# Optimization experiments

Hardware: AMD Instinct MI355X
Metric: run time of the kernel (lower is better)

The kernel has to match this reference:

```python
import jax, jax.numpy as jnp
import numpy as np

N = 4096
TOPK = 16
LEAKY = 0.2
LN_EPS = 1e-5


def _gat(x, W, a_s, a_d, b, src, dst, heads):
    # PyG-style GATConv (self-loops already included in src/dst).
    n = x.shape[0]
    h = (x @ W).reshape(n, heads, -1)                      # [N,H,F]
    e = jax.nn.leaky_relu((h * a_s).sum(-1)[src] + (h * a_d).sum(-1)[dst], LEAKY)  # [E,H]
    m = jax.ops.segment_max(e, dst, num_segments=n)        # segment softmax over dst
    p = jnp.exp(e - m[dst])
    s = jax.ops.segment_sum(p, dst, num_segments=n)
    alpha = p / s[dst]                                     # [E,H]
    out = jax.ops.segment_sum(alpha[:, :, None] * h[src], dst, num_segments=n)  # [N,H,F]
    return out.reshape(n, -1) + b


def _ln(x, g, b):
    mu = x.mean(-1, keepdims=True)
    v = ((x - mu) ** 2).mean(-1, keepdims=True)
    return (x - mu) / jnp.sqrt(v + LN_EPS) * g + b


def _transformer_layer(x, wqkv, bqkv, wo, bo, g1, b1g, w1, bb1, w2, bb2, g2, b2g, nhead):
    n, d = x.shape
    dh = d // nhead
    qkv = x @ wqkv.T + bqkv                                # [N,3d]
    q, k, v = jnp.split(qkv, 3, axis=-1)
    q = q.reshape(n, nhead, dh)
    k = k.reshape(n, nhead, dh)
    v = v.reshape(n, nhead, dh)
    scores = jnp.einsum('nhd,mhd->hnm', q, k) / jnp.sqrt(jnp.float32(dh))
    attn = jax.nn.softmax(scores, axis=-1)
    o = jnp.einsum('hnm,mhd->nhd', attn, v).reshape(n, d)
    x = _ln(x + (o @ wo.T + bo), g1, b1g)
    ff = jax.nn.relu(x @ w1 + bb1) @ w2 + bb2
    return _ln(x + ff, g2, b2g)


def _learn_graph(window, gl_w, gl_b):
    h = jnp.tanh(window @ gl_w + gl_b)                     # [N,hid]
    sim = h @ h.T                                          # [N,N]
    adj = jax.nn.relu(sim)
    masked = jnp.where(jnp.eye(N, dtype=bool), -1e9, adj)  # exclude self in top-k
    _, idx = jax.lax.top_k(masked, TOPK)                   # [N,TOPK]
    src = idx.reshape(-1)
    dst = jnp.repeat(jnp.arange(N), TOPK)
    loop = jnp.arange(N)
    return jnp.concatenate([src, loop]), jnp.concatenate([dst, loop])


def setup_inputs() -> dict:
    key = jax.random.key(0)
    ks = iter(jax.random.split(key, 64))
    def rn(shape, s=0.05):
        return jax.random.normal(next(ks), shape, jnp.float32) * s
    d = dict(
        window=rn((N, 256), 1.0),
        gl_w=rn((256, 256)), gl_b=rn((256,)),
        enc_W=rn((3, 256, 256)), enc_asrc=rn((3, 4, 64)), enc_adst=rn((3, 4, 64)), enc_b=rn((3, 256)),
        tr_wqkv=rn((2, 768, 256)), tr_bqkv=rn((2, 768)),
        tr_wo=rn((2, 256, 256)), tr_bo=rn((2, 256)),
        tr_ln1_g=jnp.ones((2, 256), jnp.float32), tr_ln1_b=jnp.zeros((2, 256), jnp.float32),
        tr_w1=rn((2, 256, 512)), tr_b1=rn((2, 512)),
        tr_w2=rn((2, 512, 256)), tr_b2=rn((2, 256)),
        tr_ln2_g=jnp.ones((2, 256), jnp.float32), tr_ln2_b=jnp.zeros((2, 256), jnp.float32),
        skip_w=rn((256, 256)), skip_b=rn((256,)),
        dec_W=rn((2, 256, 256)), dec_asrc=rn((2, 4, 64)), dec_adst=rn((2, 4, 64)), dec_b=rn((2, 256)),
        dec_lW=rn((256, 256)), dec_lasrc=rn((1, 1, 256)), dec_ladst=rn((1, 1, 256)), dec_lb=rn((256,)),
    )
    return d


def reference(window, gl_w, gl_b, enc_W, enc_asrc, enc_adst, enc_b,
              tr_wqkv, tr_bqkv, tr_wo, tr_bo, tr_ln1_g, tr_ln1_b,
              tr_w1, tr_b1, tr_w2, tr_b2, tr_ln2_g, tr_ln2_b,
              skip_w, skip_b, dec_W, dec_asrc, dec_adst, dec_b,
              dec_lW, dec_lasrc, dec_ladst, dec_lb):
    src, dst = _learn_graph(window, gl_w, gl_b)
    # encoder: 3 GAT layers with ReLU
    x = window
    for i in range(3):
        x = jax.nn.relu(_gat(x, enc_W[i], enc_asrc[i], enc_adst[i], enc_b[i], src, dst, 4))
    # transformer bottleneck (batch of 1 sequence of N tokens)
    h = x
    for i in range(2):
        h = _transformer_layer(h, tr_wqkv[i], tr_bqkv[i], tr_wo[i], tr_bo[i],
                               tr_ln1_g[i], tr_ln1_b[i], tr_w1[i], tr_b1[i],
                               tr_w2[i], tr_b2[i], tr_ln2_g[i], tr_ln2_b[i], 4)
    # skip connection
    h = h + (window @ skip_w + skip_b)
    # decoder: 2 GAT layers with ReLU, then single-head GAT
    x = h
    for i in range(2):
        x = jax.nn.relu(_gat(x, dec_W[i], dec_asrc[i], dec_adst[i], dec_b[i], src, dst, 4))
    out = _gat(x, dec_lW, dec_lasrc[0], dec_ladst[0], dec_lb, src, dst, 1)
    return out.T
```

## Files before the change

kernel.cpp:

```cpp
#include <hip/hip_runtime.h>
#include <math.h>

#define NN 4096
#define DM 256

enum { ACT_NONE = 0, ACT_RELU = 1, ACT_TANH = 2 };

typedef __attribute__((ext_vector_type(8))) short short8v;
typedef __attribute__((ext_vector_type(16))) float f32x16;

__device__ __forceinline__ unsigned short f2bf(float f) {
  unsigned int u = __float_as_uint(f);
  unsigned int r = (u + 0x7FFFu + ((u >> 16) & 1u)) >> 16;
  return (unsigned short)r;
}
__device__ __forceinline__ float bf2f(unsigned short u) {
  return __uint_as_float(((unsigned int)u) << 16);
}

__global__ __launch_bounds__(256) void cast_k(
    const float* __restrict__ src, unsigned short* __restrict__ dst, int n4) {
  const int i = blockIdx.x * 256 + threadIdx.x;
  if (i < n4) {
    const float4 v = ((const float4*)src)[i];
    ushort4 u;
    u.x = f2bf(v.x); u.y = f2bf(v.y); u.z = f2bf(v.z); u.w = f2bf(v.w);
    ((ushort4*)dst)[i] = u;
  }
}

__global__ __launch_bounds__(256) void tcast_k(
    const float* __restrict__ src, unsigned short* __restrict__ dst, int K, int N) {
  __shared__ float tile[32][33];
  const int n0 = blockIdx.x * 32, k0 = blockIdx.y * 32;
  const int tx = threadIdx.x & 31, ty = threadIdx.x >> 5;
#pragma unroll
  for (int r2 = 0; r2 < 4; r2++)
    tile[ty + r2 * 8][tx] = src[(size_t)(k0 + ty + r2 * 8) * N + n0 + tx];
  __syncthreads();
#pragma unroll
  for (int r2 = 0; r2 < 4; r2++)
    dst[(size_t)(n0 + ty + r2 * 8) * K + k0 + tx] = f2bf(tile[tx][ty + r2 * 8]);
}

__global__ __launch_bounds__(256) void split_k(
    const float* __restrict__ h, unsigned short* __restrict__ Aext,
    unsigned short* __restrict__ Bext) {
  const int n = blockIdx.x, t = threadIdx.x;
  const float v = h[(size_t)n * DM + t];
  const unsigned short hi = f2bf(v);
  const unsigned short lo = f2bf(v - bf2f(hi));
  unsigned short* ar = Aext + (size_t)n * 768;
  unsigned short* br = Bext + (size_t)n * 768;
  ar[t] = hi; ar[256 + t] = lo; ar[512 + t] = hi;
  br[t] = hi; br[256 + t] = hi; br[512 + t] = lo;
}

template<bool BT, int ACT, bool BIAS, bool RES>
__global__ __launch_bounds__(256) void gemm_k(
    const float* __restrict__ A, const float* __restrict__ B,
    const float* __restrict__ bias, const float* __restrict__ res,
    float* __restrict__ C, int M, int N, int K) {
  __shared__ float As[16][64];
  __shared__ float Bs[16][64];
  const int t = threadIdx.x;
  const int tx = t & 15, ty = t >> 4;
  const int m0 = blockIdx.y * 64, n0 = blockIdx.x * 64;
  float acc[4][4];
#pragma unroll
  for (int i = 0; i < 4; i++)
#pragma unroll
    for (int j = 0; j < 4; j++) acc[i][j] = 0.f;

  const int i_ld = t >> 2, kq = t & 3;
  for (int k0 = 0; k0 < K; k0 += 16) {
    float4 a4 = *(const float4*)(A + (size_t)(m0 + i_ld) * K + k0 + kq * 4);
    As[kq * 4 + 0][i_ld] = a4.x; As[kq * 4 + 1][i_ld] = a4.y;
    As[kq * 4 + 2][i_ld] = a4.z; As[kq * 4 + 3][i_ld] = a4.w;
    if (BT) {
      float4 b4 = *(const float4*)(B + (size_t)(n0 + i_ld) * K + k0 + kq * 4);
      Bs[kq * 4 + 0][i_ld] = b4.x; Bs[kq * 4 + 1][i_ld] = b4.y;
      Bs[kq * 4 + 2][i_ld] = b4.z; Bs[kq * 4 + 3][i_ld] = b4.w;
    } else {
      const int kk = t >> 4, j4 = (t & 15) * 4;
      float4 b4 = *(const float4*)(B + (size_t)(k0 + kk) * N + n0 + j4);
      *(float4*)&Bs[kk][j4] = b4;
    }
    __syncthreads();
#pragma unroll
    for (int kk = 0; kk < 16; kk++) {
      const float4 av = *(const float4*)&As[kk][ty * 4];
      const float4 bv = *(const float4*)&Bs[kk][tx * 4];
      acc[0][0] += av.x * bv.x; acc[0][1] += av.x * bv.y;
      acc[0][2] += av.x * bv.z; acc[0][3] += av.x * bv.w;
      acc[1][0] += av.y * bv.x; acc[1][1] += av.y * bv.y;
      acc[1][2] += av.y * bv.z; acc[1][3] += av.y * bv.w;
      acc[2][0] += av.z * bv.x; acc[2][1] += av.z * bv.y;
      acc[2][2] += av.z * bv.z; acc[2][3] += av.z * bv.w;
      acc[3][0] += av.w * bv.x; acc[3][1] += av.w * bv.y;
      acc[3][2] += av.w * bv.z; acc[3][3] += av.w * bv.w;
    }
    __syncthreads();
  }
  const int n = n0 + tx * 4;
#pragma unroll
  for (int i = 0; i < 4; i++) {
    const int m = m0 + ty * 4 + i;
    float4 v = make_float4(acc[i][0], acc[i][1], acc[i][2], acc[i][3]);
    if (BIAS) {
      v.x += bias[n + 0]; v.y += bias[n + 1];
      v.z += bias[n + 2]; v.w += bias[n + 3];
    }
    if (RES) {
      const float4 rv = *(const float4*)(res + (size_t)m * N + n);
      v.x += rv.x; v.y += rv.y; v.z += rv.z; v.w += rv.w;
    }
    if (ACT == ACT_RELU) {
      v.x = fmaxf(v.x, 0.f); v.y = fmaxf(v.y, 0.f);
      v.z = fmaxf(v.z, 0.f); v.w = fmaxf(v.w, 0.f);
    } else if (ACT == ACT_TANH) {
      v.x = tanhf(v.x); v.y = tanhf(v.y); v.z = tanhf(v.z); v.w = tanhf(v.w);
    }
    *(float4*)(C + (size_t)m * N + n) = v;
  }
}

template<int ACT, bool BIAS, bool RES, bool F32OUT, bool B16OUT>
__global__ __launch_bounds__(256) void mgemm_k(
    const unsigned short* __restrict__ A, const unsigned short* __restrict__ Bt,
    const float* __restrict__ bias, const float* __restrict__ res,
    float* __restrict__ C, unsigned short* __restrict__ Cb,
    int M, int N, int K) {
  __shared__ short As[64][64];
  __shared__ short Bs[64][64];
  const int t = threadIdx.x;
  const int m0 = blockIdx.y * 64, n0 = blockIdx.x * 64;
  const int wid = t >> 6, l = t & 63, l31 = l & 31, g = l >> 5;
  const int wm = wid >> 1, wn = wid & 1;
  f32x16 acc;
#pragma unroll
  for (int r = 0; r < 16; r++) acc[r] = 0.f;

  for (int k0 = 0; k0 < K; k0 += 64) {
#pragma unroll
    for (int p = 0; p < 2; p++) {
      const int j = p * 256 + t, row = j >> 3, ch = j & 7, sch = ch ^ (row & 7);
      *(short8v*)&As[row][sch * 8] =
          *(const short8v*)((const short*)A + (size_t)(m0 + row) * K + k0 + ch * 8);
      *(short8v*)&Bs[row][sch * 8] =
          *(const short8v*)((const short*)Bt + (size_t)(n0 + row) * K + k0 + ch * 8);
    }
    __syncthreads();
#pragma unroll
    for (int ck = 0; ck < 4; ck++) {
      const int c = ck * 2 + g;
      const short8v af = *(const short8v*)&As[wm * 32 + l31][(c ^ (l31 & 7)) * 8];
      const short8v bf = *(const short8v*)&Bs[wn * 32 + l31][(c ^ (l31 & 7)) * 8];
      acc = __builtin_amdgcn_mfma_f32_32x32x16_bf16(bf, af, acc, 0, 0, 0);
    }
    __syncthreads();
  }
  const int m = m0 + wm * 32 + l31;
#pragma unroll
  for (int b = 0; b < 4; b++) {
    const int n = n0 + wn * 32 + b * 8 + g * 4;
    float4 v = make_float4(acc[b * 4 + 0], acc[b * 4 + 1],
                           acc[b * 4 + 2], acc[b * 4 + 3]);
    if (BIAS) {
      v.x += bias[n + 0]; v.y += bias[n + 1];
      v.z += bias[n + 2]; v.w += bias[n + 3];
    }
    if (RES) {
      const float4 rv = *(const float4*)(res + (size_t)m * N + n);
      v.x += rv.x; v.y += rv.y; v.z += rv.z; v.w += rv.w;
    }
    if (ACT == ACT_RELU) {
      v.x = fmaxf(v.x, 0.f); v.y = fmaxf(v.y, 0.f);
      v.z = fmaxf(v.z, 0.f); v.w = fmaxf(v.w, 0.f);
    }
    if (F32OUT) *(float4*)(C + (size_t)m * N + n) = v;
    if (B16OUT) {
      ushort4 uv;
      uv.x = f2bf(v.x); uv.y = f2bf(v.y); uv.z = f2bf(v.z); uv.w = f2bf(v.w);
      *(ushort4*)(Cb + (size_t)m * N + n) = uv;
    }
  }
}

__global__ __launch_bounds__(256) void topk16_k(
    const float* __restrict__ sim, int* __restrict__ idxo, int rowbase) {
  const int r = blockIdx.x, t = threadIdx.x;
  const int grow = rowbase + r;
  float val[16];
#pragma unroll
  for (int q = 0; q < 16; q++) {
    const int jj = q * 256 + t;
    float v = sim[(size_t)r * NN + jj];
    v = fmaxf(v, 0.f);
    if (jj == grow) v = -1.f;
    val[q] = v;
  }
  __shared__ float cv[64];
  __shared__ int cjs[64];
  const int wave = t >> 6, lane = t & 63;
  float myv = -3.f; int myj = 0;
  for (int it = 0; it < 16; it++) {
    float bv = -10.f; int bj = 0;
#pragma unroll
    for (int q = 0; q < 16; q++)
      if (val[q] > bv) { bv = val[q]; bj = q * 256 + t; }
#pragma unroll
    for (int off = 1; off < 64; off <<= 1) {
      const float ov = __shfl_xor(bv, off);
      const int oj = __shfl_xor(bj, off);
      if (ov > bv || (ov == bv && oj < bj)) { bv = ov; bj = oj; }
    }
    if (lane == it) { myv = bv; myj = bj; }
    if ((bj & 255) == t) {
      const int q = bj >> 8;
#pragma unroll
      for (int qq = 0; qq < 16; qq++) if (qq == q) val[qq] = -2.f;
    }
  }
  if (lane < 16) { cv[wave * 16 + lane] = myv; cjs[wave * 16 + lane] = myj; }
  __syncthreads();
  if (wave == 0) {
    float bv2 = cv[lane]; int bj2 = cjs[lane];
    for (int it = 0; it < 16; it++) {
      float wv = bv2; int wj = bj2;
#pragma unroll
      for (int off = 1; off < 64; off <<= 1) {
        const float ov = __shfl_xor(wv, off);
        const int oj = __shfl_xor(wj, off);
        if (ov > wv || (ov == wv && oj < wj)) { wv = ov; wj = oj; }
      }
      if (lane == 0) idxo[(size_t)grow * 16 + it] = wj;
      if (wj == bj2) bv2 = -3.f;
    }
  }
}

template<int H>
__global__ __launch_bounds__(256) void gat_prep_k(
    const float* __restrict__ h, const float* __restrict__ as,
    const float* __restrict__ ad, float* __restrict__ es, float* __restrict__ ed) {
  __shared__ float bs[4], bd[4];
  const int n = blockIdx.x, t = threadIdx.x;
  const float v = h[(size_t)n * DM + t];
  float ps = v * as[t];
  float pd = v * ad[t];
#pragma unroll
  for (int off = 32; off >= 1; off >>= 1) {
    ps += __shfl_down(ps, off, 64);
    pd += __shfl_down(pd, off, 64);
  }
  const int wave = t >> 6, lane = t & 63;
  if (H == 4) {
    if (lane == 0) { es[n * 4 + wave] = ps; ed[n * 4 + wave] = pd; }
  } else {
    if (lane == 0) { bs[wave] = ps; bd[wave] = pd; }
    __syncthreads();
    if (t == 0) {
      es[n] = bs[0] + bs[1] + bs[2] + bs[3];
      ed[n] = bd[0] + bd[1] + bd[2] + bd[3];
    }
  }
}

template<int H, bool RELU, bool B16OUT>
__global__ __launch_bounds__(256) void gat_aggr_k(
    const float* __restrict__ h, const float* __restrict__ es,
    const float* __restrict__ ed, const int* __restrict__ idx,
    const float* __restrict__ bias, float* __restrict__ out,
    unsigned short* __restrict__ outb) {
  const int j = blockIdx.x, t = threadIdx.x;
  const int hd = (H == 4) ? (t >> 6) : 0;
  __shared__ int srcs[17];
  if (t < 16) srcs[t] = idx[(size_t)j * 16 + t];
  if (t == 16) srcs[16] = j;
  __syncthreads();
  const float edj = ed[j * H + hd];
  float e[17]; float m = -1e30f;
#pragma unroll
  for (int k = 0; k < 17; k++) {
    float ev = es[srcs[k] * H + hd] + edj;
    ev = (ev >= 0.f) ? ev : 0.2f * ev;
    e[k] = ev; m = fmaxf(m, ev);
  }
  float s = 0.f;
#pragma unroll
  for (int k = 0; k < 17; k++) { e[k] = expf(e[k] - m); s += e[k]; }
  const float inv = 1.f / s;
  float acc = 0.f;
#pragma unroll
  for (int k = 0; k < 17; k++) acc += e[k] * h[(size_t)srcs[k] * DM + t];
  acc = acc * inv + bias[t];
  if (RELU) acc = fmaxf(acc, 0.f);
  out[(size_t)j * DM + t] = acc;
  if (B16OUT) outb[(size_t)j * DM + t] = f2bf(acc);
}

__global__ __launch_bounds__(256) void vtrans_k(
    const short* __restrict__ qkvs, short* __restrict__ vt) {
  __shared__ short Vt[64][72];
  const int kb0 = blockIdx.x * 64;
  const int h = blockIdx.y;
  const int t = threadIdx.x;
  {
    const int key = t >> 2, cq = t & 3;
    const short* vp = qkvs + (size_t)(kb0 + key) * 768 + 512 + h * 64 + cq * 16;
    *(short8v*)&Vt[key][cq * 16] = *(const short8v*)(vp);
    *(short8v*)&Vt[key][cq * 16 + 8] = *(const short8v*)(vp + 8);
  }
  __syncthreads();
  const int dh = t & 63, grp = t >> 6;
  short* dst = vt + (size_t)(h * 64 + dh) * 4096 + kb0 + grp * 16;
#pragma unroll
  for (int j2 = 0; j2 < 2; j2++) {
    short8v tmp;
#pragma unroll
    for (int e = 0; e < 8; e++) {
      const int s = grp * 16 + j2 * 8 + e;
      const int w = (s & 32) | ((s & 19)) | ((s & 4) << 1) | ((s & 8) >> 1);
      tmp[e] = Vt[w][dh];
    }
    *(short8v*)(dst + j2 * 8) = tmp;
  }
}

#define LOADKV(KF, VF, KB) do {                                               \
    const short* kp_ = kbase + (size_t)((KB) + l31) * 768;                    \
    KF##0 = *(const short8v*)(kp_);                                           \
    KF##1 = *(const short8v*)(kp_ + 16);                                      \
    KF##2 = *(const short8v*)(kp_ + 32);                                      \
    KF##3 = *(const short8v*)(kp_ + 48);                                      \
    const short* vp_ = vbase + (KB);                                          \
    VF##0 = *(const short8v*)(vp_);                                           \
    VF##1 = *(const short8v*)(vp_ + 16);                                      \
    VF##2 = *(const short8v*)(vp_ + (size_t)32 * 4096);                       \
    VF##3 = *(const short8v*)(vp_ + (size_t)32 * 4096 + 16);                  \
  } while (0)

#define PROCESS(KF, VF) do {                                                  \
    f32x16 accS;                                                              \
    _Pragma("unroll") for (int r = 0; r < 16; r++) accS[r] = 0.f;             \
    __builtin_amdgcn_s_setprio(1);                                            \
    accS = __builtin_amdgcn_mfma_f32_32x32x16_bf16(KF##0, qf[0], accS, 0, 0, 0); \
    accS = __builtin_amdgcn_mfma_f32_32x32x16_bf16(KF##1, qf[1], accS, 0, 0, 0); \
    accS = __builtin_amdgcn_mfma_f32_32x32x16_bf16(KF##2, qf[2], accS, 0, 0, 0); \
    accS = __builtin_amdgcn_mfma_f32_32x32x16_bf16(KF##3, qf[3], accS, 0, 0, 0); \
    __builtin_amdgcn_s_setprio(0);                                            \
    float sv[16]; float mt = -1e30f;                                          \
    _Pragma("unroll") for (int r = 0; r < 16; r++) {                          \
      sv[r] = accS[r] * 0.18033688f;                     \
      mt = fmaxf(mt, sv[r]);                                                  \
    }                                                                         \
    mt = fmaxf(mt, __shfl_xor(mt, 32));                                       \
    float pv[16]; float ls = 0.f;                                             \
    if (__all(mt <= mrun + 11.5416f)) {                                       \
      _Pragma("unroll") for (int r = 0; r < 16; r++) {                        \
        pv[r] = exp2f(sv[r] - mrun); ls += pv[r];                             \
      }                                                                       \
      ls += __shfl_xor(ls, 32); lrun += ls;                                   \
    } else {                                                                  \
      const float mnew = fmaxf(mrun, mt);                                     \
      const float corr = exp2f(mrun - mnew);                                  \
      _Pragma("unroll") for (int r = 0; r < 16; r++) {                        \
        pv[r] = exp2f(sv[r] - mnew); ls += pv[r];                             \
      }                                                                       \
      ls += __shfl_xor(ls, 32);                                               \
      lrun = lrun * corr + ls; mrun = mnew;                                   \
      _Pragma("unroll") for (int r = 0; r < 16; r++) {                        \
        accO[0][r] *= corr; accO[1][r] *= corr;                               \
      }                                                                       \
    }                                                                         \
    union { unsigned int u[8]; short8v s[2]; } pf;                            \
    _Pragma("unroll") for (int r = 0; r < 8; r++) {                           \
      unsigned int po;                                                        \
      asm("v_cvt_pk_bf16_f32 %0, %1, %2"                                      \
          : "=v"(po) : "v"(pv[2 * r]), "v"(pv[2 * r + 1]));                   \
      pf.u[r] = po;                                                           \
    }                                                                         \
    __builtin_amdgcn_s_setprio(1);                                            \
    accO[0] = __builtin_amdgcn_mfma_f32_32x32x16_bf16(VF##0, pf.s[0], accO[0], 0, 0, 0); \
    accO[0] = __builtin_amdgcn_mfma_f32_32x32x16_bf16(VF##1, pf.s[1], accO[0], 0, 0, 0); \
    accO[1] = __builtin_amdgcn_mfma_f32_32x32x16_bf16(VF##2, pf.s[0], accO[1], 0, 0, 0); \
    accO[1] = __builtin_amdgcn_mfma_f32_32x32x16_bf16(VF##3, pf.s[1], accO[1], 0, 0, 0); \
    __builtin_amdgcn_s_setprio(0);                                            \
  } while (0)

__global__ __launch_bounds__(64) void attn_flash_k(
    const short* __restrict__ qkvs, const short* __restrict__ vt,
    unsigned short* __restrict__ opart, float* __restrict__ ml) {
  const int qb = blockIdx.x * 32;
  const int h = blockIdx.y;
  const int z = blockIdx.z;
  const int l = threadIdx.x;
  const int l31 = l & 31, g = l >> 5;

  short8v qf[4];
  {
    const short* qp = qkvs + (size_t)(qb + l31) * 768 + h * 64 + g * 8;
#pragma unroll
    for (int c = 0; c < 4; c++) qf[c] = *(const short8v*)(qp + c * 16);
  }

  f32x16 accO[2];
#pragma unroll
  for (int r = 0; r < 16; r++) { accO[0][r] = 0.f; accO[1][r] = 0.f; }
  float mrun = -1e30f, lrun = 0.f;

  const short* kbase = qkvs + 256 + h * 64 + g * 8;
  const short* vbase = vt + (size_t)(h * 64 + l31) * 4096 + g * 8;
  const int kb0 = z * 1024;

  short8v kA0, kA1, kA2, kA3, vA0, vA1, vA2, vA3;
  short8v kB0, kB1, kB2, kB3, vB0, vB1, vB2, vB3;
  LOADKV(kA, vA, kb0);
  for (int it = 0; it < 16; it++) {
    LOADKV(kB, vB, kb0 + (it * 2 + 1) * 32);
    PROCESS(kA, vA);
    LOADKV(kA, vA, kb0 + ((it * 2 + 2) & 31) * 32);
    PROCESS(kB, vB);
  }

  const int q = qb + l31;
  unsigned short* op = opart + ((size_t)z * NN + q) * DM + h * 64;
#pragma unroll
  for (int db = 0; db < 2; db++) {
#pragma unroll
    for (int rq = 0; rq < 4; rq++) {
      ushort4 v4;
      v4.x = f2bf(accO[db][rq * 4 + 0]);
      v4.y = f2bf(accO[db][rq * 4 + 1]);
      v4.z = f2bf(accO[db][rq * 4 + 2]);
      v4.w = f2bf(accO[db][rq * 4 + 3]);
      *(ushort4*)(op + db * 32 + rq * 8 + g * 4) = v4;
    }
  }
  if (g == 0) {
    ml[(((size_t)z * 4 + h) * NN + q) * 2 + 0] = mrun;
    ml[(((size_t)z * 4 + h) * NN + q) * 2 + 1] = lrun;
  }
}

__global__ __launch_bounds__(256) void attn_merge_k(
    const unsigned short* __restrict__ opart, const float* __restrict__ ml,
    unsigned short* __restrict__ ob) {
  const int q = blockIdx.x;
  const int t = threadIdx.x;
  const int h = t >> 6;
  float m[4], lv[4];
#pragma unroll
  for (int z = 0; z < 4; z++) {
    m[z]  = ml[(((size_t)z * 4 + h) * NN + q) * 2 + 0];
    lv[z] = ml[(((size_t)z * 4 + h) * NN + q) * 2 + 1];
  }
  const float ms = fmaxf(fmaxf(m[0], m[1]), fmaxf(m[2], m[3]));
  float w[4]; float ls = 0.f;
#pragma unroll
  for (int z = 0; z < 4; z++) {
    w[z] = exp2f(m[z] - ms);
    ls += lv[z] * w[z];
  }
  const float inv = 1.f / ls;
  float acc = 0.f;
#pragma unroll
  for (int z = 0; z < 4; z++)
    acc += bf2f(opart[((size_t)z * NN + q) * DM + t]) * w[z];
  ob[(size_t)q * DM + t] = f2bf(acc * inv);
}

__global__ __launch_bounds__(256) void ln_k(
    const float* __restrict__ x, const float* __restrict__ g,
    const float* __restrict__ b, float* __restrict__ y,
    unsigned short* __restrict__ yb) {
  __shared__ float bs[4], bs2[4];
  const int n = blockIdx.x, t = threadIdx.x;
  const float v = x[(size_t)n * DM + t];
  float s = v, s2 = v * v;
#pragma unroll
  for (int off = 32; off >= 1; off >>= 1) {
    s += __shfl_down(s, off, 64);
    s2 += __shfl_down(s2, off, 64);
  }
  const int wave = t >> 6, lane = t & 63;
  if (lane == 0) { bs[wave] = s; bs2[wave] = s2; }
  __syncthreads();
  const float ts = bs[0] + bs[1] + bs[2] + bs[3];
  const float ts2 = bs2[0] + bs2[1] + bs2[2] + bs2[3];
  const float mu = ts * (1.f / 256.f);
  const float var = ts2 * (1.f / 256.f) - mu * mu;
  const float rstd = 1.f / sqrtf(var + 1e-5f);
  const float o = (v - mu) * rstd * g[t] + b[t];
  y[(size_t)n * DM + t] = o;
  yb[(size_t)n * DM + t] = f2bf(o);
}

__global__ __launch_bounds__(1024) void transpose_k(
    const float* __restrict__ x, float* __restrict__ out) {
  __shared__ float tile[32][33];
  const int n0 = blockIdx.x * 32, c0 = blockIdx.y * 32;
  const int tx = threadIdx.x, ty = threadIdx.y;
  tile[ty][tx] = x[(size_t)(n0 + ty) * DM + c0 + tx];
  __syncthreads();
  out[(size_t)(c0 + ty) * NN + n0 + tx] = tile[tx][ty];
}

extern "C" void kernel_launch(void* const* d_in, const int* in_sizes, int n_in,
                              void* d_out, int out_size, void* d_ws, size_t ws_size,
                              hipStream_t stream) {
  (void)in_sizes; (void)n_in; (void)out_size; (void)ws_size;
  const float* window   = (const float*)d_in[0];
  const float* gl_w     = (const float*)d_in[1];
  const float* gl_b     = (const float*)d_in[2];
  const float* enc_W    = (const float*)d_in[3];
  const float* enc_asrc = (const float*)d_in[4];
  const float* enc_adst = (const float*)d_in[5];
  const float* enc_b    = (const float*)d_in[6];
  const float* tr_wqkv  = (const float*)d_in[7];
  const float* tr_bqkv  = (const float*)d_in[8];
  const float* tr_wo    = (const float*)d_in[9];
  const float* tr_bo    = (const float*)d_in[10];
  const float* tr_ln1_g = (const float*)d_in[11];
  const float* tr_ln1_b = (const float*)d_in[12];
  const float* tr_w1    = (const float*)d_in[13];
  const float* tr_b1    = (const float*)d_in[14];
  const float* tr_w2    = (const float*)d_in[15];
  const float* tr_b2    = (const float*)d_in[16];
  const float* tr_ln2_g = (const float*)d_in[17];
  const float* tr_ln2_b = (const float*)d_in[18];
  const float* skip_w   = (const float*)d_in[19];
  const float* skip_b   = (const float*)d_in[20];
  const float* dec_W    = (const float*)d_in[21];
  const float* dec_asrc = (const float*)d_in[22];
  const float* dec_adst = (const float*)d_in[23];
  const float* dec_b    = (const float*)d_in[24];
  const float* dec_lW   = (const float*)d_in[25];
  const float* dec_lasrc= (const float*)d_in[26];
  const float* dec_ladst= (const float*)d_in[27];
  const float* dec_lb   = (const float*)d_in[28];
  float* outp = (float*)d_out;

  float* ws   = (float*)d_ws;
  float* xa   = ws;
  float* xb   = ws + 1048576;
  float* hp   = ws + 2097152;
  float* t1   = ws + 3145728;
  float* hgl  = t1;
  float* mlb  = t1;
  float* qkvb = ws + 4194304;
  float* vtb  = ws + 5767168;
  float* Rg   = ws + 6291456;
  float* simc = Rg;
  unsigned short* opartb = (unsigned short*)Rg;
  unsigned short* ffb    = (unsigned short*)Rg;
  float* es   = ws + 8388608;
  float* ed   = ws + 8404992;
  int*   idx  = (int*)(ws + 8421376);
  unsigned short* winb = (unsigned short*)(ws + 8486912);
  unsigned short* actb = (unsigned short*)(ws + 9011200);
  unsigned short* wb   = (unsigned short*)(ws + 9535488);

  unsigned short* encWt = wb;
  unsigned short* wqkvb = wb + 196608;
  unsigned short* wob   = wb + 589824;
  unsigned short* w1t   = wb + 720896;
  unsigned short* w2t   = wb + 983040;
  unsigned short* skipt = wb + 1245184;
  unsigned short* dect  = wb + 1310720;
  unsigned short* declt = wb + 1441792;

  unsigned short* Aext = (unsigned short*)qkvb;
  unsigned short* Bext = (unsigned short*)xa;

  const dim3 B256(256);

  cast_k<<<dim3(1024), B256, 0, stream>>>(window, winb, 262144);
  for (int i = 0; i < 3; i++)
    tcast_k<<<dim3(8, 8), B256, 0, stream>>>(enc_W + (size_t)i * 65536, encWt + (size_t)i * 65536, 256, 256);
  cast_k<<<dim3(384), B256, 0, stream>>>(tr_wqkv, wqkvb, 98304);
  cast_k<<<dim3(128), B256, 0, stream>>>(tr_wo, wob, 32768);
  for (int i = 0; i < 2; i++) {
    tcast_k<<<dim3(16, 8), B256, 0, stream>>>(tr_w1 + (size_t)i * 131072, w1t + (size_t)i * 131072, 256, 512);
    tcast_k<<<dim3(8, 16), B256, 0, stream>>>(tr_w2 + (size_t)i * 131072, w2t + (size_t)i * 131072, 512, 256);
    tcast_k<<<dim3(8, 8), B256, 0, stream>>>(dec_W + (size_t)i * 65536, dect + (size_t)i * 65536, 256, 256);
  }
  tcast_k<<<dim3(8, 8), B256, 0, stream>>>(skip_w, skipt, 256, 256);
  tcast_k<<<dim3(8, 8), B256, 0, stream>>>(dec_lW, declt, 256, 256);

  gemm_k<false, ACT_TANH, true, false><<<dim3(DM / 64, NN / 64), B256, 0, stream>>>(
      window, gl_w, gl_b, nullptr, hgl, NN, DM, DM);

  split_k<<<dim3(NN), B256, 0, stream>>>(hgl, Aext, Bext);
  for (int c = 0; c < 8; c++) {
    mgemm_k<ACT_NONE, false, false, true, false><<<dim3(64, 8), B256, 0, stream>>>(
        Aext + (size_t)c * 512 * 768, Bext, nullptr, nullptr, simc, nullptr,
        512, NN, 768);
    topk16_k<<<dim3(512), B256, 0, stream>>>(simc, idx, c * 512);
  }

  for (int i = 0; i < 3; i++) {
    const unsigned short* ain = (i == 0) ? winb : actb;
    mgemm_k<ACT_NONE, false, false, true, false><<<dim3(4, 64), B256, 0, stream>>>(
        ain, encWt + (size_t)i * 65536, nullptr, nullptr, hp, nullptr, NN, DM, DM);
    gat_prep_k<4><<<dim3(NN), B256, 0, stream>>>(hp, enc_asrc + i * 256, enc_adst + i * 256, es, ed);
    gat_aggr_k<4, true, true><<<dim3(NN), B256, 0, stream>>>(
        hp, es, ed, idx, enc_b + i * 256, xa, actb);
  }

  for (int i = 0; i < 2; i++) {
    mgemm_k<ACT_NONE, true, false, false, true><<<dim3(12, 64), B256, 0, stream>>>(
        actb, wqkvb + (size_t)i * 196608, tr_bqkv + i * 768, nullptr,
        nullptr, (unsigned short*)qkvb, NN, 768, DM);
    vtrans_k<<<dim3(64, 4), B256, 0, stream>>>((const short*)qkvb, (short*)vtb);
    attn_flash_k<<<dim3(NN / 32, 4, 4), dim3(64), 0, stream>>>(
        (const short*)qkvb, (const short*)vtb, opartb, mlb);
    attn_merge_k<<<dim3(NN), B256, 0, stream>>>(opartb, mlb, actb);
    mgemm_k<ACT_NONE, true, true, true, false><<<dim3(4, 64), B256, 0, stream>>>(
        actb, wob + (size_t)i * 65536, tr_bo + i * 256, xa, t1, nullptr, NN, DM, DM);
    ln_k<<<dim3(NN), B256, 0, stream>>>(t1, tr_ln1_g + i * 256, tr_ln1_b + i * 256, xb, actb);
    mgemm_k<ACT_RELU, true, false, false, true><<<dim3(8, 64), B256, 0, stream>>>(
        actb, w1t + (size_t)i * 131072, tr_b1 + i * 512, nullptr,
        nullptr, ffb, NN, 512, DM);
    mgemm_k<ACT_NONE, true, true, true, false><<<dim3(4, 64), B256, 0, stream>>>(
        ffb, w2t + (size_t)i * 131072, tr_b2 + i * 256, xb, t1, nullptr, NN, DM, 512);
    ln_k<<<dim3(NN), B256, 0, stream>>>(t1, tr_ln2_g + i * 256, tr_ln2_b + i * 256, xa, actb);
  }

  mgemm_k<ACT_NONE, true, true, false, true><<<dim3(4, 64), B256, 0, stream>>>(
      winb, skipt, skip_b, xa, nullptr, actb, NN, DM, DM);

  mgemm_k<ACT_NONE, false, false, true, false><<<dim3(4, 64), B256, 0, stream>>>(
      actb, dect, nullptr, nullptr, hp, nullptr, NN, DM, DM);
  gat_prep_k<4><<<dim3(NN), B256, 0, stream>>>(hp, dec_asrc, dec_adst, es, ed);
  gat_aggr_k<4, true, true><<<dim3(NN), B256, 0, stream>>>(hp, es, ed, idx, dec_b, xb, actb);

  mgemm_k<ACT_NONE, false, false, true, false><<<dim3(4, 64), B256, 0, stream>>>(
      actb, dect + 65536, nullptr, nullptr, hp, nullptr, NN, DM, DM);
  gat_prep_k<4><<<dim3(NN), B256, 0, stream>>>(hp, dec_asrc + 256, dec_adst + 256, es, ed);
  gat_aggr_k<4, true, true><<<dim3(NN), B256, 0, stream>>>(hp, es, ed, idx, dec_b + 256, xb, actb);

  mgemm_k<ACT_NONE, false, false, true, false><<<dim3(4, 64), B256, 0, stream>>>(
      actb, declt, nullptr, nullptr, hp, nullptr, NN, DM, DM);
  gat_prep_k<1><<<dim3(NN), B256, 0, stream>>>(hp, dec_lasrc, dec_ladst, es, ed);
  gat_aggr_k<1, false, false><<<dim3(NN), B256, 0, stream>>>(hp, es, ed, idx, dec_lb, xa, nullptr);

  transpose_k<<<dim3(NN / 32, DM / 32), dim3(32, 32), 0, stream>>>(xa, outp);
}
```

Measured before the change: 857.0 us.

## Merge flash-attention split-K partials in shared memory and batch weight casts

The attention kernel now runs 8 waves per block, each handling a 512-key slice, and merges their partial outputs and softmax stats through shared memory. This removes the separate merge kernel and the global round trip of the bf16 partials. The softmax scale is folded into Q when it is loaded, which drops a multiply per score but rounds the scaled Q to bf16 once more. The many cast/transpose launches for weights are also batched into two launches. The cost is heavier shared-memory use and block-wide synchronisation inside the attention kernel.

```diff
diff --git a/kernel.cpp b/kernel.cpp
--- a/kernel.cpp
+++ b/kernel.cpp
@@ -18,29 +18,33 @@
   return __uint_as_float(((unsigned int)u) << 16);
 }
 
-__global__ __launch_bounds__(256) void cast_k(
-    const float* __restrict__ src, unsigned short* __restrict__ dst, int n4) {
+struct CastJob { const float* s; unsigned short* d; int n4; };
+__global__ __launch_bounds__(256) void castall_k(CastJob j0, CastJob j1, CastJob j2) {
+  const CastJob* jp = (blockIdx.y == 0) ? &j0 : (blockIdx.y == 1) ? &j1 : &j2;
   const int i = blockIdx.x * 256 + threadIdx.x;
-  if (i < n4) {
-    const float4 v = ((const float4*)src)[i];
+  if (i < jp->n4) {
+    const float4 v = ((const float4*)jp->s)[i];
     ushort4 u;
     u.x = f2bf(v.x); u.y = f2bf(v.y); u.z = f2bf(v.z); u.w = f2bf(v.w);
-    ((ushort4*)dst)[i] = u;
-  }
-}
-
-__global__ __launch_bounds__(256) void tcast_k(
-    const float* __restrict__ src, unsigned short* __restrict__ dst, int K, int N) {
+    ((ushort4*)jp->d)[i] = u;
+  }
+}
+
+struct TJob { const float* s; unsigned short* d; int K; int N; };
+struct TJobs { TJob j[11]; };
+__global__ __launch_bounds__(256) void tcastall_k(TJobs js) {
+  const TJob jb = js.j[blockIdx.z];
+  const int n0 = blockIdx.x * 32, k0 = blockIdx.y * 32;
+  if (n0 >= jb.N || k0 >= jb.K) return;
   __shared__ float tile[32][33];
-  const int n0 = blockIdx.x * 32, k0 = blockIdx.y * 32;
   const int tx = threadIdx.x & 31, ty = threadIdx.x >> 5;
 #pragma unroll
   for (int r2 = 0; r2 < 4; r2++)
-    tile[ty + r2 * 8][tx] = src[(size_t)(k0 + ty + r2 * 8) * N + n0 + tx];
+    tile[ty + r2 * 8][tx] = jb.s[(size_t)(k0 + ty + r2 * 8) * jb.N + n0 + tx];
   __syncthreads();
 #pragma unroll
   for (int r2 = 0; r2 < 4; r2++)
-    dst[(size_t)(n0 + ty + r2 * 8) * K + k0 + tx] = f2bf(tile[tx][ty + r2 * 8]);
+    jb.d[(size_t)(n0 + ty + r2 * 8) * jb.K + k0 + tx] = f2bf(tile[tx][ty + r2 * 8]);
 }
 
 __global__ __launch_bounds__(256) void split_k(
@@ -350,23 +354,20 @@
     accS = __builtin_amdgcn_mfma_f32_32x32x16_bf16(KF##2, qf[2], accS, 0, 0, 0); \
     accS = __builtin_amdgcn_mfma_f32_32x32x16_bf16(KF##3, qf[3], accS, 0, 0, 0); \
     __builtin_amdgcn_s_setprio(0);                                            \
-    float sv[16]; float mt = -1e30f;                                          \
-    _Pragma("unroll") for (int r = 0; r < 16; r++) {                          \
-      sv[r] = accS[r] * 0.18033688f;                     \
-      mt = fmaxf(mt, sv[r]);                                                  \
-    }                                                                         \
+    float mt = -1e30f;                                                        \
+    _Pragma("unroll") for (int r = 0; r < 16; r++) mt = fmaxf(mt, accS[r]);   \
     mt = fmaxf(mt, __shfl_xor(mt, 32));                                       \
     float pv[16]; float ls = 0.f;                                             \
     if (__all(mt <= mrun + 11.5416f)) {                                       \
       _Pragma("unroll") for (int r = 0; r < 16; r++) {                        \
-        pv[r] = exp2f(sv[r] - mrun); ls += pv[r];                             \
+        pv[r] = exp2f(accS[r] - mrun); ls += pv[r];                           \
       }                                                                       \
       ls += __shfl_xor(ls, 32); lrun += ls;                                   \
     } else {                                                                  \
       const float mnew = fmaxf(mrun, mt);                                     \
       const float corr = exp2f(mrun - mnew);                                  \
       _Pragma("unroll") for (int r = 0; r < 16; r++) {                        \
-        pv[r] = exp2f(sv[r] - mnew); ls += pv[r];                             \
+        pv[r] = exp2f(accS[r] - mnew); ls += pv[r];                           \
       }                                                                       \
       ls += __shfl_xor(ls, 32);                                               \
       lrun = lrun * corr + ls; mrun = mnew;                                   \
@@ -389,20 +390,30 @@
     __builtin_amdgcn_s_setprio(0);                                            \
   } while (0)
 
-__global__ __launch_bounds__(64) void attn_flash_k(
+__global__ __launch_bounds__(512, 4) void attn_flash_k(
     const short* __restrict__ qkvs, const short* __restrict__ vt,
-    unsigned short* __restrict__ opart, float* __restrict__ ml) {
+    unsigned short* __restrict__ ob) {
   const int qb = blockIdx.x * 32;
   const int h = blockIdx.y;
-  const int z = blockIdx.z;
-  const int l = threadIdx.x;
+  const int t = threadIdx.x;
+  const int w = t >> 6;
+  const int l = t & 63;
   const int l31 = l & 31, g = l >> 5;
+
+  __shared__ float smem[8][32][66];
+  __shared__ float sml[8][32][2];
 
   short8v qf[4];
   {
     const short* qp = qkvs + (size_t)(qb + l31) * 768 + h * 64 + g * 8;
 #pragma unroll
-    for (int c = 0; c < 4; c++) qf[c] = *(const short8v*)(qp + c * 16);
+    for (int c = 0; c < 4; c++) {
+      short8v qv = *(const short8v*)(qp + c * 16);
+#pragma unroll
+      for (int e = 0; e < 8; e++)
+        qv[e] = (short)f2bf(bf2f((unsigned short)qv[e]) * 0.18033688f);
+      qf[c] = qv;
+    }
   }
 
   f32x16 accO[2];
@@ -412,63 +423,53 @@
 
   const short* kbase = qkvs + 256 + h * 64 + g * 8;
   const short* vbase = vt + (size_t)(h * 64 + l31) * 4096 + g * 8;
-  const int kb0 = z * 1024;
+  const int kb0 = w * 512;
 
   short8v kA0, kA1, kA2, kA3, vA0, vA1, vA2, vA3;
   short8v kB0, kB1, kB2, kB3, vB0, vB1, vB2, vB3;
   LOADKV(kA, vA, kb0);
-  for (int it = 0; it < 16; it++) {
+  for (int it = 0; it < 8; it++) {
     LOADKV(kB, vB, kb0 + (it * 2 + 1) * 32);
     PROCESS(kA, vA);
-    LOADKV(kA, vA, kb0 + ((it * 2 + 2) & 31) * 32);
+    LOADKV(kA, vA, kb0 + ((it * 2 + 2) & 15) * 32);
     PROCESS(kB, vB);
   }
 
-  const int q = qb + l31;
-  unsigned short* op = opart + ((size_t)z * NN + q) * DM + h * 64;
-#pragma unroll
-  for (int db = 0; db < 2; db++) {
-#pragma unroll
-    for (int rq = 0; rq < 4; rq++) {
-      ushort4 v4;
-      v4.x = f2bf(accO[db][rq * 4 + 0]);
-      v4.y = f2bf(accO[db][rq * 4 + 1]);
-      v4.z = f2bf(accO[db][rq * 4 + 2]);
-      v4.w = f2bf(accO[db][rq * 4 + 3]);
-      *(ushort4*)(op + db * 32 + rq * 8 + g * 4) = v4;
-    }
-  }
-  if (g == 0) {
-    ml[(((size_t)z * 4 + h) * NN + q) * 2 + 0] = mrun;
-    ml[(((size_t)z * 4 + h) * NN + q) * 2 + 1] = lrun;
-  }
-}
-
-__global__ __launch_bounds__(256) void attn_merge_k(
-    const unsigned short* __restrict__ opart, const float* __restrict__ ml,
-    unsigned short* __restrict__ ob) {
-  const int q = blockIdx.x;
-  const int t = threadIdx.x;
-  const int h = t >> 6;
-  float m[4], lv[4];
-#pragma unroll
-  for (int z = 0; z < 4; z++) {
-    m[z]  = ml[(((size_t)z * 4 + h) * NN + q) * 2 + 0];
-    lv[z] = ml[(((size_t)z * 4 + h) * NN + q) * 2 + 1];
-  }
-  const float ms = fmaxf(fmaxf(m[0], m[1]), fmaxf(m[2], m[3]));
-  float w[4]; float ls = 0.f;
-#pragma unroll
-  for (int z = 0; z < 4; z++) {
-    w[z] = exp2f(m[z] - ms);
-    ls += lv[z] * w[z];
-  }
-  const float inv = 1.f / ls;
-  float acc = 0.f;
-#pragma unroll
-  for (int z = 0; z < 4; z++)
-    acc += bf2f(opart[((size_t)z * NN + q) * DM + t]) * w[z];
-  ob[(size_t)q * DM + t] = f2bf(acc * inv);
+  if (g == 0) { sml[w][l31][0] = mrun; sml[w][l31][1] = lrun; }
+  __syncthreads();
+  float M = sml[0][l31][0];
+#pragma unroll
+  for (int ww = 1; ww < 8; ww++) M = fmaxf(M, sml[ww][l31][0]);
+  const float wgt = exp2f(mrun - M);
+#pragma unroll
+  for (int db = 0; db < 2; db++)
+#pragma unroll
+    for (int r = 0; r < 16; r++) {
+      const int dh = db * 32 + (r & 3) + 8 * (r >> 2) + 4 * g;
+      smem[w][l31][dh] = accO[db][r] * wgt;
+    }
+  __syncthreads();
+  const int q = t >> 4, d4 = (t & 15) * 4;
+  float M2 = sml[0][q][0];
+#pragma unroll
+  for (int ww = 1; ww < 8; ww++) M2 = fmaxf(M2, sml[ww][q][0]);
+  float lsum = 0.f;
+#pragma unroll
+  for (int ww = 0; ww < 8; ww++)
+    lsum += sml[ww][q][1] * exp2f(sml[ww][q][0] - M2);
+  float o0 = 0.f, o1 = 0.f, o2 = 0.f, o3 = 0.f;
+#pragma unroll
+  for (int ww = 0; ww < 8; ww++) {
+    o0 += smem[ww][q][d4 + 0];
+    o1 += smem[ww][q][d4 + 1];
+    o2 += smem[ww][q][d4 + 2];
+    o3 += smem[ww][q][d4 + 3];
+  }
+  const float inv = 1.f / lsum;
+  ushort4 uv;
+  uv.x = f2bf(o0 * inv); uv.y = f2bf(o1 * inv);
+  uv.z = f2bf(o2 * inv); uv.w = f2bf(o3 * inv);
+  *(ushort4*)(ob + (size_t)(qb + q) * DM + h * 64 + d4) = uv;
 }
 
 __global__ __launch_bounds__(256) void ln_k(
@@ -548,13 +549,11 @@
   float* hp   = ws + 2097152;
   float* t1   = ws + 3145728;
   float* hgl  = t1;
-  float* mlb  = t1;
   float* qkvb = ws + 4194304;
   float* vtb  = ws + 5767168;
   float* Rg   = ws + 6291456;
   float* simc = Rg;
-  unsigned short* opartb = (unsigned short*)Rg;
-  unsigned short* ffb    = (unsigned short*)Rg;
+  unsigned short* ffb = (unsigned short*)Rg;
   float* es   = ws + 8388608;
   float* ed   = ws + 8404992;
   int*   idx  = (int*)(ws + 8421376);
@@ -576,18 +575,20 @@
 
   const dim3 B256(256);
 
-  cast_k<<<dim3(1024), B256, 0, stream>>>(window, winb, 262144);
-  for (int i = 0; i < 3; i++)
-    tcast_k<<<dim3(8, 8), B256, 0, stream>>>(enc_W + (size_t)i * 65536, encWt + (size_t)i * 65536, 256, 256);
-  cast_k<<<dim3(384), B256, 0, stream>>>(tr_wqkv, wqkvb, 98304);
-  cast_k<<<dim3(128), B256, 0, stream>>>(tr_wo, wob, 32768);
-  for (int i = 0; i < 2; i++) {
-    tcast_k<<<dim3(16, 8), B256, 0, stream>>>(tr_w1 + (size_t)i * 131072, w1t + (size_t)i * 131072, 256, 512);
-    tcast_k<<<dim3(8, 16), B256, 0, stream>>>(tr_w2 + (size_t)i * 131072, w2t + (size_t)i * 131072, 512, 256);
-    tcast_k<<<dim3(8, 8), B256, 0, stream>>>(dec_W + (size_t)i * 65536, dect + (size_t)i * 65536, 256, 256);
-  }
-  tcast_k<<<dim3(8, 8), B256, 0, stream>>>(skip_w, skipt, 256, 256);
-  tcast_k<<<dim3(8, 8), B256, 0, stream>>>(dec_lW, declt, 256, 256);
+  {
+    CastJob c0{window, winb, 262144};
+    CastJob c1{tr_wqkv, wqkvb, 98304};
+    CastJob c2{tr_wo, wob, 32768};
+    castall_k<<<dim3(1024, 3), B256, 0, stream>>>(c0, c1, c2);
+    TJobs tj;
+    for (int i = 0; i < 3; i++) tj.j[i] = {enc_W + (size_t)i * 65536, encWt + (size_t)i * 65536, 256, 256};
+    for (int i = 0; i < 2; i++) tj.j[3 + i] = {tr_w1 + (size_t)i * 131072, w1t + (size_t)i * 131072, 256, 512};
+    for (int i = 0; i < 2; i++) tj.j[5 + i] = {tr_w2 + (size_t)i * 131072, w2t + (size_t)i * 131072, 512, 256};
+    tj.j[7] = {skip_w, skipt, 256, 256};
+    for (int i = 0; i < 2; i++) tj.j[8 + i] = {dec_W + (size_t)i * 65536, dect + (size_t)i * 65536, 256, 256};
+    tj.j[10] = {dec_lW, declt, 256, 256};
+    tcastall_k<<<dim3(16, 16, 11), B256, 0, stream>>>(tj);
+  }
 
   gemm_k<false, ACT_TANH, true, false><<<dim3(DM / 64, NN / 64), B256, 0, stream>>>(
       window, gl_w, gl_b, nullptr, hgl, NN, DM, DM);
@@ -614,9 +615,8 @@
         actb, wqkvb + (size_t)i * 196608, tr_bqkv + i * 768, nullptr,
         nullptr, (unsigned short*)qkvb, NN, 768, DM);
     vtrans_k<<<dim3(64, 4), B256, 0, stream>>>((const short*)qkvb, (short*)vtb);
-    attn_flash_k<<<dim3(NN / 32, 4, 4), dim3(64), 0, stream>>>(
-        (const short*)qkvb, (const short*)vtb, opartb, mlb);
-    attn_merge_k<<<dim3(NN), B256, 0, stream>>>(opartb, mlb, actb);
+    attn_flash_k<<<dim3(NN / 32, 4), dim3(512), 0, stream>>>(
+        (const short*)qkvb, (const short*)vtb, actb);
     mgemm_k<ACT_NONE, true, true, true, false><<<dim3(4, 64), B256, 0, stream>>>(
         actb, wob + (size_t)i * 65536, tr_bo + i * 256, xa, t1, nullptr, NN, DM, DM);
     ln_k<<<dim3(NN), B256, 0, stream>>>(t1, tr_ln1_g + i * 256, tr_ln1_b + i * 256, xb, actb);
```

Result: slower. 1.163 ms (+35.6%).

## Pre-pack K/V into MFMA fragment layout, fold softmax scale into Q, batch casts

Applied to the files above, without the earlier changes.

Replaces the V-transpose kernel with a kernel that writes both K and V into the exact per-lane MFMA fragment order. Each attention load then becomes a contiguous 512-element-strided read instead of a 768-stride row gather. The softmax scale is folded into Q at load time, which removes a multiply per score element. The many weight cast and transpose launches are merged into two batched kernels to cut launch overhead. Rounding the pre-scaled Q to bf16 slightly changes numerics, and the fragment buffers reuse the hp workspace.

```diff
diff --git a/kernel.cpp b/kernel.cpp
--- a/kernel.cpp
+++ b/kernel.cpp
@@ -18,29 +18,33 @@
   return __uint_as_float(((unsigned int)u) << 16);
 }
 
-__global__ __launch_bounds__(256) void cast_k(
-    const float* __restrict__ src, unsigned short* __restrict__ dst, int n4) {
+struct CastJob { const float* s; unsigned short* d; int n4; };
+__global__ __launch_bounds__(256) void castall_k(CastJob j0, CastJob j1, CastJob j2) {
+  const CastJob* jp = (blockIdx.y == 0) ? &j0 : (blockIdx.y == 1) ? &j1 : &j2;
   const int i = blockIdx.x * 256 + threadIdx.x;
-  if (i < n4) {
-    const float4 v = ((const float4*)src)[i];
+  if (i < jp->n4) {
+    const float4 v = ((const float4*)jp->s)[i];
     ushort4 u;
     u.x = f2bf(v.x); u.y = f2bf(v.y); u.z = f2bf(v.z); u.w = f2bf(v.w);
-    ((ushort4*)dst)[i] = u;
-  }
-}
-
-__global__ __launch_bounds__(256) void tcast_k(
-    const float* __restrict__ src, unsigned short* __restrict__ dst, int K, int N) {
+    ((ushort4*)jp->d)[i] = u;
+  }
+}
+
+struct TJob { const float* s; unsigned short* d; int K; int N; };
+struct TJobs { TJob j[11]; };
+__global__ __launch_bounds__(256) void tcastall_k(TJobs js) {
+  const TJob jb = js.j[blockIdx.z];
+  const int n0 = blockIdx.x * 32, k0 = blockIdx.y * 32;
+  if (n0 >= jb.N || k0 >= jb.K) return;
   __shared__ float tile[32][33];
-  const int n0 = blockIdx.x * 32, k0 = blockIdx.y * 32;
   const int tx = threadIdx.x & 31, ty = threadIdx.x >> 5;
 #pragma unroll
   for (int r2 = 0; r2 < 4; r2++)
-    tile[ty + r2 * 8][tx] = src[(size_t)(k0 + ty + r2 * 8) * N + n0 + tx];
+    tile[ty + r2 * 8][tx] = jb.s[(size_t)(k0 + ty + r2 * 8) * jb.N + n0 + tx];
   __syncthreads();
 #pragma unroll
   for (int r2 = 0; r2 < 4; r2++)
-    dst[(size_t)(n0 + ty + r2 * 8) * K + k0 + tx] = f2bf(tile[tx][ty + r2 * 8]);
+    jb.d[(size_t)(n0 + ty + r2 * 8) * jb.K + k0 + tx] = f2bf(tile[tx][ty + r2 * 8]);
 }
 
 __global__ __launch_bounds__(256) void split_k(
@@ -300,45 +304,53 @@
   if (B16OUT) outb[(size_t)j * DM + t] = f2bf(acc);
 }
 
-__global__ __launch_bounds__(256) void vtrans_k(
-    const short* __restrict__ qkvs, short* __restrict__ vt) {
-  __shared__ short Vt[64][72];
-  const int kb0 = blockIdx.x * 64;
+__global__ __launch_bounds__(256) void kvfrag_k(
+    const short* __restrict__ qkvs, short* __restrict__ kf,
+    short* __restrict__ vf) {
+  const int kc = blockIdx.x;
   const int h = blockIdx.y;
   const int t = threadIdx.x;
+  __shared__ short Ks[32][72];
+  __shared__ short Vs[32][72];
   {
-    const int key = t >> 2, cq = t & 3;
-    const short* vp = qkvs + (size_t)(kb0 + key) * 768 + 512 + h * 64 + cq * 16;
-    *(short8v*)&Vt[key][cq * 16] = *(const short8v*)(vp);
-    *(short8v*)&Vt[key][cq * 16 + 8] = *(const short8v*)(vp + 8);
+    const int row = t >> 3, ch = t & 7;
+    const short* kp = qkvs + (size_t)(kc * 32 + row) * 768 + 256 + h * 64 + ch * 8;
+    *(short8v*)&Ks[row][ch * 8] = *(const short8v*)kp;
+    const short* vp = qkvs + (size_t)(kc * 32 + row) * 768 + 512 + h * 64 + ch * 8;
+    *(short8v*)&Vs[row][ch * 8] = *(const short8v*)vp;
   }
   __syncthreads();
-  const int dh = t & 63, grp = t >> 6;
-  short* dst = vt + (size_t)(h * 64 + dh) * 4096 + kb0 + grp * 16;
-#pragma unroll
-  for (int j2 = 0; j2 < 2; j2++) {
-    short8v tmp;
+  {
+    const int dc = t >> 6, l = t & 63, l31 = l & 31, g = l >> 5;
+    short8v kv;
+#pragma unroll
+    for (int e = 0; e < 8; e++) kv[e] = Ks[l31][dc * 16 + g * 8 + e];
+    *(short8v*)(kf + ((size_t)(h * 128 + kc) * 4 + dc) * 512 + l * 8) = kv;
+  }
+  {
+    const int db = t >> 7, kg = (t >> 6) & 1, l = t & 63, l31 = l & 31, g = l >> 5;
+    short8v vv;
 #pragma unroll
     for (int e = 0; e < 8; e++) {
-      const int s = grp * 16 + j2 * 8 + e;
-      const int w = (s & 32) | ((s & 19)) | ((s & 4) << 1) | ((s & 8) >> 1);
-      tmp[e] = Vt[w][dh];
-    }
-    *(short8v*)(dst + j2 * 8) = tmp;
-  }
-}
-
-#define LOADKV(KF, VF, KB) do {                                               \
-    const short* kp_ = kbase + (size_t)((KB) + l31) * 768;                    \
+      const int j = kg * 16 + g * 8 + e;
+      const int jp = (j & 19) | ((j & 4) << 1) | ((j & 8) >> 1);
+      vv[e] = Vs[jp][db * 32 + l31];
+    }
+    *(short8v*)(vf + (((size_t)(h * 128 + kc) * 2 + db) * 2 + kg) * 512 + l * 8) = vv;
+  }
+}
+
+#define LOADKV(KF, VF, KC) do {                                               \
+    const short* kp_ = kfrag + ((size_t)(KC)) * 2048 + l * 8;                 \
     KF##0 = *(const short8v*)(kp_);                                           \
-    KF##1 = *(const short8v*)(kp_ + 16);                                      \
-    KF##2 = *(const short8v*)(kp_ + 32);                                      \
-    KF##3 = *(const short8v*)(kp_ + 48);                                      \
-    const short* vp_ = vbase + (KB);                                          \
+    KF##1 = *(const short8v*)(kp_ + 512);                                     \
+    KF##2 = *(const short8v*)(kp_ + 1024);                                    \
+    KF##3 = *(const short8v*)(kp_ + 1536);                                    \
+    const short* vp_ = vfrag + ((size_t)(KC)) * 2048 + l * 8;                 \
     VF##0 = *(const short8v*)(vp_);                                           \
-    VF##1 = *(const short8v*)(vp_ + 16);                                      \
-    VF##2 = *(const short8v*)(vp_ + (size_t)32 * 4096);                       \
-    VF##3 = *(const short8v*)(vp_ + (size_t)32 * 4096 + 16);                  \
+    VF##1 = *(const short8v*)(vp_ + 512);                                     \
+    VF##2 = *(const short8v*)(vp_ + 1024);                                    \
+    VF##3 = *(const short8v*)(vp_ + 1536);                                    \
   } while (0)
 
 #define PROCESS(KF, VF) do {                                                  \
@@ -350,23 +362,20 @@
     accS = __builtin_amdgcn_mfma_f32_32x32x16_bf16(KF##2, qf[2], accS, 0, 0, 0); \
     accS = __builtin_amdgcn_mfma_f32_32x32x16_bf16(KF##3, qf[3], accS, 0, 0, 0); \
     __builtin_amdgcn_s_setprio(0);                                            \
-    float sv[16]; float mt = -1e30f;                                          \
-    _Pragma("unroll") for (int r = 0; r < 16; r++) {                          \
-      sv[r] = accS[r] * 0.18033688f;                     \
-      mt = fmaxf(mt, sv[r]);                                                  \
-    }                                                                         \
+    float mt = -1e30f;                                                        \
+    _Pragma("unroll") for (int r = 0; r < 16; r++) mt = fmaxf(mt, accS[r]);   \
     mt = fmaxf(mt, __shfl_xor(mt, 32));                                       \
     float pv[16]; float ls = 0.f;                                             \
     if (__all(mt <= mrun + 11.5416f)) {                                       \
       _Pragma("unroll") for (int r = 0; r < 16; r++) {                        \
-        pv[r] = exp2f(sv[r] - mrun); ls += pv[r];                             \
+        pv[r] = exp2f(accS[r] - mrun); ls += pv[r];                           \
       }                                                                       \
       ls += __shfl_xor(ls, 32); lrun += ls;                                   \
     } else {                                                                  \
       const float mnew = fmaxf(mrun, mt);                                     \
       const float corr = exp2f(mrun - mnew);                                  \
       _Pragma("unroll") for (int r = 0; r < 16; r++) {                        \
-        pv[r] = exp2f(sv[r] - mnew); ls += pv[r];                             \
+        pv[r] = exp2f(accS[r] - mnew); ls += pv[r];                           \
       }                                                                       \
       ls += __shfl_xor(ls, 32);                                               \
       lrun = lrun * corr + ls; mrun = mnew;                                   \
@@ -390,8 +399,9 @@
   } while (0)
 
 __global__ __launch_bounds__(64) void attn_flash_k(
-    const short* __restrict__ qkvs, const short* __restrict__ vt,
-    unsigned short* __restrict__ opart, float* __restrict__ ml) {
+    const short* __restrict__ qkvs, const short* __restrict__ kfb,
+    const short* __restrict__ vfb, unsigned short* __restrict__ opart,
+    float* __restrict__ ml) {
   const int qb = blockIdx.x * 32;
   const int h = blockIdx.y;
   const int z = blockIdx.z;
@@ -402,7 +412,13 @@
   {
     const short* qp = qkvs + (size_t)(qb + l31) * 768 + h * 64 + g * 8;
 #pragma unroll
-    for (int c = 0; c < 4; c++) qf[c] = *(const short8v*)(qp + c * 16);
+    for (int c = 0; c < 4; c++) {
+      short8v qv = *(const short8v*)(qp + c * 16);
+#pragma unroll
+      for (int e = 0; e < 8; e++)
+        qv[e] = (short)f2bf(bf2f((unsigned short)qv[e]) * 0.18033688f);
+      qf[c] = qv;
+    }
   }
 
   f32x16 accO[2];
@@ -410,17 +426,17 @@
   for (int r = 0; r < 16; r++) { accO[0][r] = 0.f; accO[1][r] = 0.f; }
   float mrun = -1e30f, lrun = 0.f;
 
-  const short* kbase = qkvs + 256 + h * 64 + g * 8;
-  const short* vbase = vt + (size_t)(h * 64 + l31) * 4096 + g * 8;
-  const int kb0 = z * 1024;
+  const short* kfrag = kfb + (size_t)h * 128 * 2048;
+  const short* vfrag = vfb + (size_t)h * 128 * 2048;
+  const int kc0 = z * 32;
 
   short8v kA0, kA1, kA2, kA3, vA0, vA1, vA2, vA3;
   short8v kB0, kB1, kB2, kB3, vB0, vB1, vB2, vB3;
-  LOADKV(kA, vA, kb0);
+  LOADKV(kA, vA, kc0);
   for (int it = 0; it < 16; it++) {
-    LOADKV(kB, vB, kb0 + (it * 2 + 1) * 32);
+    LOADKV(kB, vB, kc0 + (it * 2 + 1));
     PROCESS(kA, vA);
-    LOADKV(kA, vA, kb0 + ((it * 2 + 2) & 31) * 32);
+    LOADKV(kA, vA, kc0 + ((it * 2 + 2) & 31));
     PROCESS(kB, vB);
   }
 
@@ -550,7 +566,6 @@
   float* hgl  = t1;
   float* mlb  = t1;
   float* qkvb = ws + 4194304;
-  float* vtb  = ws + 5767168;
   float* Rg   = ws + 6291456;
   float* simc = Rg;
   unsigned short* opartb = (unsigned short*)Rg;
@@ -574,20 +589,25 @@
   unsigned short* Aext = (unsigned short*)qkvb;
   unsigned short* Bext = (unsigned short*)xa;
 
+  short* kfb = (short*)hp;
+  short* vfb = (short*)hp + 1048576;
+
   const dim3 B256(256);
 
-  cast_k<<<dim3(1024), B256, 0, stream>>>(window, winb, 262144);
-  for (int i = 0; i < 3; i++)
-    tcast_k<<<dim3(8, 8), B256, 0, stream>>>(enc_W + (size_t)i * 65536, encWt + (size_t)i * 65536, 256, 256);
-  cast_k<<<dim3(384), B256, 0, stream>>>(tr_wqkv, wqkvb, 98304);
-  cast_k<<<dim3(128), B256, 0, stream>>>(tr_wo, wob, 32768);
-  for (int i = 0; i < 2; i++) {
-    tcast_k<<<dim3(16, 8), B256, 0, stream>>>(tr_w1 + (size_t)i * 131072, w1t + (size_t)i * 131072, 256, 512);
-    tcast_k<<<dim3(8, 16), B256, 0, stream>>>(tr_w2 + (size_t)i * 131072, w2t + (size_t)i * 131072, 512, 256);
-    tcast_k<<<dim3(8, 8), B256, 0, stream>>>(dec_W + (size_t)i * 65536, dect + (size_t)i * 65536, 256, 256);
-  }
-  tcast_k<<<dim3(8, 8), B256, 0, stream>>>(skip_w, skipt, 256, 256);
-  tcast_k<<<dim3(8, 8), B256, 0, stream>>>(dec_lW, declt, 256, 256);
+  {
+    CastJob c0{window, winb, 262144};
+    CastJob c1{tr_wqkv, wqkvb, 98304};
+    CastJob c2{tr_wo, wob, 32768};
+    castall_k<<<dim3(1024, 3), B256, 0, stream>>>(c0, c1, c2);
+    TJobs tj;
+    for (int i = 0; i < 3; i++) tj.j[i] = {enc_W + (size_t)i * 65536, encWt + (size_t)i * 65536, 256, 256};
+    for (int i = 0; i < 2; i++) tj.j[3 + i] = {tr_w1 + (size_t)i * 131072, w1t + (size_t)i * 131072, 256, 512};
+    for (int i = 0; i < 2; i++) tj.j[5 + i] = {tr_w2 + (size_t)i * 131072, w2t + (size_t)i * 131072, 512, 256};
+    tj.j[7] = {skip_w, skipt, 256, 256};
+    for (int i = 0; i < 2; i++) tj.j[8 + i] = {dec_W + (size_t)i * 65536, dect + (size_t)i * 65536, 256, 256};
+    tj.j[10] = {dec_lW, declt, 256, 256};
+    tcastall_k<<<dim3(16, 16, 11), B256, 0, stream>>>(tj);
+  }
 
   gemm_k<false, ACT_TANH, true, false><<<dim3(DM / 64, NN / 64), B256, 0, stream>>>(
       window, gl_w, gl_b, nullptr, hgl, NN, DM, DM);
@@ -613,9 +633,9 @@
     mgemm_k<ACT_NONE, true, false, false, true><<<dim3(12, 64), B256, 0, stream>>>(
         actb, wqkvb + (size_t)i * 196608, tr_bqkv + i * 768, nullptr,
         nullptr, (unsigned short*)qkvb, NN, 768, DM);
-    vtrans_k<<<dim3(64, 4), B256, 0, stream>>>((const short*)qkvb, (short*)vtb);
+    kvfrag_k<<<dim3(128, 4), B256, 0, stream>>>((const short*)qkvb, kfb, vfb);
     attn_flash_k<<<dim3(NN / 32, 4, 4), dim3(64), 0, stream>>>(
-        (const short*)qkvb, (const short*)vtb, opartb, mlb);
+        (const short*)qkvb, kfb, vfb, opartb, mlb);
     attn_merge_k<<<dim3(NN), B256, 0, stream>>>(opartb, mlb, actb);
     mgemm_k<ACT_NONE, true, true, true, false><<<dim3(4, 64), B256, 0, stream>>>(
         actb, wob + (size_t)i * 65536, tr_bo + i * 256, xa, t1, nullptr, NN, DM, DM);
```

Result: faster. 780.9 us (-8.9%).
